# Kernel tuning notes

Hardware: AMD Instinct MI355X
Metric: run time of the kernel (lower is better)

Reference implementation:

```python
import jax, jax.numpy as jnp
import numpy as np

B, H, W, C = 1, 72, 72, 768
NH, HD = 12, 64
FF = 3072
EPS = 1e-6
THETA = 10000.0
S = H * W


def _rope_tables():
    freqs = 1.0 / THETA ** (np.arange(0, HD, 4, dtype=np.float32) / HD)  # [16]
    t = np.arange(H, dtype=np.float32)
    fx = np.outer(t, freqs)  # [72,16]
    fy = np.outer(t, freqs)
    fx = np.tile(fx[:, None, :], (1, W, 1))  # [72,72,16]
    fy = np.tile(fy[None, :, :], (H, 1, 1))
    fxy = np.concatenate([fx, fy], axis=-1).reshape(S, -1)  # [5184,32]
    fxy = np.repeat(fxy, 2, axis=-1)  # [5184,64]
    return jnp.asarray(np.cos(fxy)), jnp.asarray(np.sin(fxy))


def _rotate_pairwise(x):
    x1 = x[..., ::2]
    x2 = x[..., 1::2]
    return jnp.stack([-x2, x1], axis=-1).reshape(x.shape)


def _layernorm(x, g, b):
    m = jnp.mean(x, axis=-1, keepdims=True)
    v = jnp.mean(jnp.square(x - m), axis=-1, keepdims=True)
    return (x - m) * jax.lax.rsqrt(v + EPS) * g + b


def setup_inputs() -> dict:
    key = jax.random.key(0)
    ks = jax.random.split(key, 12)
    s_c = 1.0 / np.sqrt(C)
    s_ff = 1.0 / np.sqrt(FF)
    d = {
        "hidden_states": jax.random.normal(ks[0], (B, H, W, C), jnp.float32),
        "wq": jax.random.normal(ks[1], (C, C), jnp.float32) * s_c,
        "bq": jnp.zeros((C,), jnp.float32),
        "wk": jax.random.normal(ks[2], (C, C), jnp.float32) * s_c,
        "bk": jnp.zeros((C,), jnp.float32),
        "wv": jax.random.normal(ks[3], (C, C), jnp.float32) * s_c,
        "bv": jnp.zeros((C,), jnp.float32),
        "wo": jax.random.normal(ks[4], (C, C), jnp.float32) * s_c,
        "bo": jnp.zeros((C,), jnp.float32),
        "g1": jnp.ones((C,), jnp.float32),
        "b1": jnp.zeros((C,), jnp.float32),
        "g2": jnp.ones((C,), jnp.float32),
        "b2": jnp.zeros((C,), jnp.float32),
        "w_fc1": jax.random.normal(ks[5], (C, FF), jnp.float32) * s_c,
        "b_fc1": jnp.zeros((FF,), jnp.float32),
        "w_fc2": jax.random.normal(ks[6], (FF, C), jnp.float32) * s_ff,
        "b_fc2": jnp.zeros((C,), jnp.float32),
        "ls1": jnp.full((C,), 1e-5, jnp.float32),
        "ls2": jnp.full((C,), 1e-5, jnp.float32),
    }
    return d


def reference(hidden_states, wq, bq, wk, bk, wv, bv, wo, bo, g1, b1, g2, b2,
              w_fc1, b_fc1, w_fc2, b_fc2, ls1, ls2):
    cos, sin = _rope_tables()  # [S, HD]
    cos = cos[None, None]  # [1,1,S,HD]
    sin = sin[None, None]

    residual = hidden_states
    x = hidden_states.reshape(B, S, C)
    x = _layernorm(x, g1, b1)

    # attention
    q = (x @ wq + bq).reshape(B, S, NH, HD).transpose(0, 2, 1, 3)
    k = (x @ wk + bk).reshape(B, S, NH, HD).transpose(0, 2, 1, 3)
    v = (x @ wv + bv).reshape(B, S, NH, HD).transpose(0, 2, 1, 3)
    q = q * cos + _rotate_pairwise(q) * sin
    k = k * cos + _rotate_pairwise(k) * sin
    scale = HD ** -0.5
    attn = jax.nn.softmax(jnp.einsum('bhqd,bhkd->bhqk', q, k) * scale, axis=-1)
    o = jnp.einsum('bhqk,bhkd->bhqd', attn, v)
    o = o.transpose(0, 2, 1, 3).reshape(B, S, C)
    o = o @ wo + bo
    o = o * ls1

    hs = residual + o.reshape(B, H, W, C)
    residual = hs
    x = _layernorm(hs.reshape(B, S, C), g2, b2)
    x = jax.nn.gelu(x @ w_fc1 + b_fc1, approximate=False)
    x = x @ w_fc2 + b_fc2
    x = x * ls2
    return residual + x.reshape(B, H, W, C)
```

## Files before the change

### kernel.cpp

```cpp
#include <hip/hip_runtime.h>

#define S_  5184
#define C_  768
#define NH_ 12
#define HD_ 64
#define FF_ 3072
#define WW_ 72

typedef __attribute__((ext_vector_type(8))) short bf16x8;
typedef __attribute__((ext_vector_type(4))) float f32x4;

__device__ __forceinline__ float bf2f(unsigned short u){
    unsigned int i = ((unsigned int)u) << 16; float f; __builtin_memcpy(&f,&i,4); return f;
}
__device__ __forceinline__ unsigned short f2bf(float f){
    unsigned int i; __builtin_memcpy(&i,&f,4);
    unsigned int r = (i + 0x7fffu + ((i>>16)&1u)) >> 16;
    return (unsigned short)r;
}
__device__ __forceinline__ float ldf(float v){ return v; }
__device__ __forceinline__ float ldf(unsigned short v){ return bf2f(v); }

__device__ __forceinline__ void gload16(const void* g, const void* l) {
    __builtin_amdgcn_global_load_lds((const __attribute__((address_space(1))) void*)g,
                                     (__attribute__((address_space(3))) void*)l, 16, 0, 0);
}
__device__ __forceinline__ unsigned int cvtpk(float lo, float hi){
    unsigned int r;
    asm volatile("v_cvt_pk_bf16_f32 %0, %1, %2" : "=v"(r) : "v"(lo), "v"(hi));
    return r;
}

template<typename TIN>
__global__ __launch_bounds__(256) void ln_k(const TIN* __restrict__ x,
                                            const float* __restrict__ g,
                                            const float* __restrict__ b,
                                            unsigned short* __restrict__ out)
{
    int row = blockIdx.x, tid = threadIdx.x;
    const TIN* xr = x + (size_t)row * C_;
    float v0 = ldf(xr[tid]), v1 = ldf(xr[tid+256]), v2 = ldf(xr[tid+512]);
    float s = v0+v1+v2, q = v0*v0+v1*v1+v2*v2;
    #pragma unroll
    for (int off=32; off; off>>=1){ s += __shfl_xor(s,off); q += __shfl_xor(q,off); }
    __shared__ float ss[4], qq[4], mshare[2];
    int lane = tid & 63, wv = tid >> 6;
    if (!lane){ ss[wv] = s; qq[wv] = q; }
    __syncthreads();
    if (!tid){
        float S2 = ss[0]+ss[1]+ss[2]+ss[3];
        float Q2 = qq[0]+qq[1]+qq[2]+qq[3];
        float mean = S2 * (1.f/C_);
        float var  = Q2 * (1.f/C_) - mean*mean;
        mshare[0] = mean; mshare[1] = rsqrtf(var + 1e-6f);
    }
    __syncthreads();
    float mean = mshare[0], inv = mshare[1];
    unsigned short* orow = out + (size_t)row * C_;
    orow[tid]     = f2bf((v0-mean)*inv*g[tid]     + b[tid]);
    orow[tid+256] = f2bf((v1-mean)*inv*g[tid+256] + b[tid+256]);
    orow[tid+512] = f2bf((v2-mean)*inv*g[tid+512] + b[tid+512]);
}

__global__ __launch_bounds__(256) void rope_tables_k(float* __restrict__ cosT,
                                                     float* __restrict__ sinT)
{
    int idx = blockIdx.x * 256 + threadIdx.x;
    if (idx >= S_*32) return;
    int s = idx >> 5, i = idx & 31;
    int hh = s / WW_, ww = s % WW_;
    int m = i & 15;
    float coord = (i < 16) ? (float)hh : (float)ww;
    float freq = powf(10000.0f, -(float)m / 16.0f);
    float a = coord * freq;
    float c = cosf(a), sn = sinf(a);
    cosT[s*64 + 2*i]   = c;  cosT[s*64 + 2*i+1] = c;
    sinT[s*64 + 2*i]   = sn; sinT[s*64 + 2*i+1] = sn;
}

__global__ __launch_bounds__(256) void rope_apply_k(unsigned short* __restrict__ q,
                                                    unsigned short* __restrict__ k,
                                                    const float* __restrict__ cosT,
                                                    const float* __restrict__ sinT)
{
    int idx = blockIdx.x * 256 + threadIdx.x;
    if (idx >= S_*NH_*32) return;
    int s = idx / (NH_*32);
    int p = idx % (NH_*32);
    int h = p >> 5, i = p & 31;
    size_t base = (size_t)s*C_ + h*HD_ + 2*i;
    float c = cosT[s*64 + 2*i], sn = sinT[s*64 + 2*i];
    float x0 = bf2f(q[base]), x1 = bf2f(q[base+1]);
    q[base]   = f2bf((x0*c - x1*sn) * 0.125f);
    q[base+1] = f2bf((x1*c + x0*sn) * 0.125f);
    x0 = bf2f(k[base]); x1 = bf2f(k[base+1]);
    k[base]   = f2bf(x0*c - x1*sn);
    k[base+1] = f2bf(x1*c + x0*sn);
}

__global__ __launch_bounds__(256) void transpose_w(const float* __restrict__ W,
                                                   unsigned short* __restrict__ WT,
                                                   int K, int N)
{
    __shared__ float t[32][33];
    int tx = threadIdx.x, ty = threadIdx.y;
    int n0 = blockIdx.x * 32, k0 = blockIdx.y * 32;
    #pragma unroll
    for (int i = 0; i < 4; i++)
        t[ty + i*8][tx] = W[(size_t)(k0 + ty + i*8)*N + n0 + tx];
    __syncthreads();
    #pragma unroll
    for (int i = 0; i < 4; i++)
        WT[(size_t)(n0 + ty + i*8)*K + k0 + tx] = f2bf(t[tx][ty + i*8]);
}

template<int EPI, int NWC>
__global__ __launch_bounds__(256) void gemm_mfma(const unsigned short* __restrict__ A,
                                                 const unsigned short* __restrict__ BT,
                                                 const float* __restrict__ bias,
                                                 const float* __restrict__ biasB,
                                                 const float* __restrict__ biasC,
                                                 const float* __restrict__ scale,
                                                 const float* __restrict__ addend,
                                                 void* __restrict__ outp,
                                                 void* __restrict__ outp2,
                                                 int M, int N, int K)
{
    const int BN = 64*NWC;
    const int MI = (NWC == 2) ? 4 : 2;
    __shared__ __align__(16) unsigned short As[2][8192];
    __shared__ __align__(16) unsigned short Bs[2][4096*NWC];
    int tid = threadIdx.x;
    int w = tid >> 6, lane = tid & 63, lq = lane & 15, lk = lane >> 4;
    int wr = (NWC == 2) ? (w >> 1) : w;
    int wc = (NWC == 2) ? (w & 1) : 0;
    int bm = blockIdx.y * 128, bn = blockIdx.x * BN;

    f32x4 acc[MI][4];
    #pragma unroll
    for (int i = 0; i < MI; i++)
        #pragma unroll
        for (int j = 0; j < 4; j++) acc[i][j] = 0;

    auto STAGE = [&](int buf, int kt) {
        #pragma unroll
        for (int u = 0; u < 4; u++) {
            int t = w*4 + u;
            int c = t*64 + lane;
            int kg = c >> 7, row = c & 127;
            int ra = bm + row; if (ra >= M) ra = M - 1;
            gload16(A + (size_t)ra*K + kt*64 + kg*8, As[buf] + t*512);
        }
        #pragma unroll
        for (int u = 0; u < 2*NWC; u++) {
            int t = w*2*NWC + u;
            int c = t*64 + lane;
            int kg = (NWC == 2) ? (c >> 7) : (c >> 6);
            int row = (NWC == 2) ? (c & 127) : (c & 63);
            gload16(BT + (size_t)(bn + row)*K + kt*64 + kg*8, Bs[buf] + t*512);
        }
    };

    int nk = K / 64;
    STAGE(0, 0);
    int cur = 0;
    for (int kt = 0; kt < nk; kt++) {
        __syncthreads();
        if (kt + 1 < nk) STAGE(cur ^ 1, kt + 1);
        #pragma unroll
        for (int kk = 0; kk < 2; kk++) {
            bf16x8 af[MI], bfr[4];
            #pragma unroll
            for (int mi = 0; mi < MI; mi++)
                af[mi] = *(const bf16x8*)(As[cur] + (kk*4 + lk)*1024 + (wr*MI*16 + mi*16 + lq)*8);
            #pragma unroll
            for (int ni = 0; ni < 4; ni++)
                bfr[ni] = *(const bf16x8*)(Bs[cur] + (kk*4 + lk)*BN*8 + (wc*64 + ni*16 + lq)*8);
            #pragma unroll
            for (int mi = 0; mi < MI; mi++)
                #pragma unroll
                for (int ni = 0; ni < 4; ni++)
                    acc[mi][ni] = __builtin_amdgcn_mfma_f32_16x16x32_bf16(af[mi], bfr[ni], acc[mi][ni], 0, 0, 0);
        }
        cur ^= 1;
    }

    #pragma unroll
    for (int mi = 0; mi < MI; mi++) {
        #pragma unroll
        for (int ni = 0; ni < 4; ni++) {
            int n = bn + wc*64 + ni*16 + lq;
            int m0 = bm + wr*MI*16 + mi*16 + lk*4;
            if (EPI == 4) {
                if (n < 1536) {
                    const float* bb = (n < 768) ? bias : biasB;
                    int nn = (n < 768) ? n : (n - 768);
                    size_t base = (n < 768) ? 0 : ((size_t)S_ * 768);
                    #pragma unroll
                    for (int r = 0; r < 4; r++) {
                        int m = m0 + r;
                        if (m < M)
                            ((unsigned short*)outp)[base + (size_t)m*768 + nn] = f2bf(acc[mi][ni][r] + bb[nn]);
                    }
                } else {
                    if (m0 < M) {
                        float bv = biasC[n - 1536];
                        ushort4 pv;
                        pv.x = f2bf(acc[mi][ni][0] + bv);
                        pv.y = f2bf(acc[mi][ni][1] + bv);
                        pv.z = f2bf(acc[mi][ni][2] + bv);
                        pv.w = f2bf(acc[mi][ni][3] + bv);
                        *(ushort4*)((unsigned short*)outp2 + (size_t)(n - 1536)*S_ + m0) = pv;
                    }
                }
            } else {
                #pragma unroll
                for (int r = 0; r < 4; r++) {
                    int m = m0 + r;
                    if (m < M) {
                        float v = acc[mi][ni][r] + bias[n];
                        if (EPI == 1) {
                            v = 0.5f * v * (1.f + erff(v * 0.70710678f));
                            ((unsigned short*)outp)[(size_t)m*N + n] = f2bf(v);
                        } else {
                            size_t o = (size_t)m*N + n;
                            ((float*)outp)[o] = v*scale[n] + addend[o];
                        }
                    }
                }
            }
        }
    }
}

__global__ __launch_bounds__(256) void attn_mfma2(const unsigned short* __restrict__ Q,
                                                  const unsigned short* __restrict__ Kb,
                                                  const unsigned short* __restrict__ Vt,
                                                  unsigned short* __restrict__ O)
{
    __shared__ __align__(16) unsigned short Ks[2][4096];
    __shared__ __align__(16) unsigned short Vs[2][4096];
    int tid = threadIdx.x;
    int w = tid >> 6, lane = tid & 63, lq = lane & 15, lk = lane >> 4;
    int h = blockIdx.y;
    int q0 = blockIdx.x * 128 + w * 32;

    bf16x8 qf[2][2];
    #pragma unroll
    for (int qi = 0; qi < 2; qi++) {
        int qr = q0 + qi*16 + lq; if (qr >= S_) qr = S_ - 1;
        #pragma unroll
        for (int ks = 0; ks < 2; ks++)
            qf[qi][ks] = *(const bf16x8*)(Q + (size_t)qr*C_ + h*64 + ks*32 + lk*8);
    }

    f32x4 oacc[2][4];
    #pragma unroll
    for (int qi = 0; qi < 2; qi++)
        #pragma unroll
        for (int df = 0; df < 4; df++) oacc[qi][df] = 0;
    float m_[2] = {-INFINITY, -INFINITY};
    float l_[2] = {0.f, 0.f};

    auto STAGE = [&](int buf, int t) {
        int kv0 = t * 64;
        #pragma unroll
        for (int u = 0; u < 4; u++) {
            int tt = w*4 + u;
            if (tt < 8)
                gload16(Kb + (size_t)(kv0 + lane)*C_ + h*64 + tt*8, Ks[buf] + tt*512);
            else
                gload16(Vt + (size_t)(h*64 + lane)*S_ + kv0 + (tt-8)*8, Vs[buf] + (tt-8)*512);
        }
    };

    const int NT = S_/64;
    STAGE(0, 0);
    int cur = 0;
    for (int t = 0; t < NT; t++) {
        __syncthreads();
        if (t + 1 < NT) STAGE(cur ^ 1, t + 1);

        f32x4 s[2][4];
        #pragma unroll
        for (int qi = 0; qi < 2; qi++)
            #pragma unroll
            for (int nf = 0; nf < 4; nf++) s[qi][nf] = 0;
        #pragma unroll
        for (int ks = 0; ks < 2; ks++) {
            #pragma unroll
            for (int nf = 0; nf < 4; nf++) {
                bf16x8 kf = *(const bf16x8*)(Ks[cur] + (ks*4 + lk)*512 + (nf*16 + lq)*8);
                #pragma unroll
                for (int qi = 0; qi < 2; qi++)
                    s[qi][nf] = __builtin_amdgcn_mfma_f32_16x16x32_bf16(kf, qf[qi][ks], s[qi][nf], 0, 0, 0);
            }
        }

        unsigned int pk[2][8];
        #pragma unroll
        for (int qi = 0; qi < 2; qi++) {
            float tm = -INFINITY;
            #pragma unroll
            for (int nf = 0; nf < 4; nf++)
                #pragma unroll
                for (int r = 0; r < 4; r++) tm = fmaxf(tm, s[qi][nf][r]);
            tm = fmaxf(tm, __shfl_xor(tm, 16));
            tm = fmaxf(tm, __shfl_xor(tm, 32));
            float mn = fmaxf(m_[qi], tm);
            float corr = __expf(m_[qi] - mn);
            m_[qi] = mn;
            float ps = 0.f;
            #pragma unroll
            for (int nf = 0; nf < 4; nf++)
                #pragma unroll
                for (int r = 0; r < 4; r++) {
                    float p = __expf(s[qi][nf][r] - mn);
                    s[qi][nf][r] = p; ps += p;
                }
            ps += __shfl_xor(ps, 16);
            ps += __shfl_xor(ps, 32);
            l_[qi] = l_[qi]*corr + ps;
            #pragma unroll
            for (int df = 0; df < 4; df++)
                #pragma unroll
                for (int r = 0; r < 4; r++) oacc[qi][df][r] *= corr;
            #pragma unroll
            for (int nf = 0; nf < 4; nf++) {
                pk[qi][nf*2+0] = cvtpk(s[qi][nf][0], s[qi][nf][1]);
                pk[qi][nf*2+1] = cvtpk(s[qi][nf][2], s[qi][nf][3]);
            }
        }

        #pragma unroll
        for (int ks = 0; ks < 2; ks++) {
            #pragma unroll
            for (int df = 0; df < 4; df++) {
                int d = df*16 + lq;
                union { bf16x8 v; unsigned long long dd[2]; } va;
                va.dd[0] = *(const unsigned long long*)(Vs[cur] + (4*ks + (lk>>1))*512 + d*8 + (lk&1)*4);
                va.dd[1] = *(const unsigned long long*)(Vs[cur] + (4*ks + 2 + (lk>>1))*512 + d*8 + (lk&1)*4);
                #pragma unroll
                for (int qi = 0; qi < 2; qi++) {
                    union { bf16x8 v; unsigned int u[4]; } pb;
                    pb.u[0] = pk[qi][4*ks+0]; pb.u[1] = pk[qi][4*ks+1];
                    pb.u[2] = pk[qi][4*ks+2]; pb.u[3] = pk[qi][4*ks+3];
                    oacc[qi][df] = __builtin_amdgcn_mfma_f32_16x16x32_bf16(va.v, pb.v, oacc[qi][df], 0, 0, 0);
                }
            }
        }
        cur ^= 1;
    }

    #pragma unroll
    for (int qi = 0; qi < 2; qi++) {
        int q = q0 + qi*16 + lq;
        if (q < S_) {
            float rl = 1.f / l_[qi];
            #pragma unroll
            for (int df = 0; df < 4; df++) {
                ushort4 pv;
                pv.x = f2bf(oacc[qi][df][0] * rl);
                pv.y = f2bf(oacc[qi][df][1] * rl);
                pv.z = f2bf(oacc[qi][df][2] * rl);
                pv.w = f2bf(oacc[qi][df][3] * rl);
                *(ushort4*)(O + (size_t)q*C_ + h*64 + df*16 + lk*4) = pv;
            }
        }
    }
}

extern "C" void kernel_launch(void* const* d_in, const int* in_sizes, int n_in,
                              void* d_out, int out_size, void* d_ws, size_t ws_size,
                              hipStream_t stream)
{
    const float* hidden = (const float*)d_in[0];
    const float* wq  = (const float*)d_in[1];
    const float* bq  = (const float*)d_in[2];
    const float* wk  = (const float*)d_in[3];
    const float* bk  = (const float*)d_in[4];
    const float* wv  = (const float*)d_in[5];
    const float* bv  = (const float*)d_in[6];
    const float* wo  = (const float*)d_in[7];
    const float* bo  = (const float*)d_in[8];
    const float* g1  = (const float*)d_in[9];
    const float* b1  = (const float*)d_in[10];
    const float* g2  = (const float*)d_in[11];
    const float* b2  = (const float*)d_in[12];
    const float* wf1 = (const float*)d_in[13];
    const float* bf1 = (const float*)d_in[14];
    const float* wf2 = (const float*)d_in[15];
    const float* bf2_ = (const float*)d_in[16];
    const float* ls1 = (const float*)d_in[17];
    const float* ls2 = (const float*)d_in[18];

    char* ws = (char*)d_ws;
    size_t off = 0;
    auto alloc = [&](size_t bytes) { char* p = ws + off; off += (bytes + 255) & ~(size_t)255; return p; };

    float* res1          = (float*)alloc((size_t)S_*C_*4);
    float* cosT          = (float*)alloc((size_t)S_*64*4);
    float* sinT          = (float*)alloc((size_t)S_*64*4);
    unsigned short* lnb  = (unsigned short*)alloc((size_t)S_*C_*2);
    unsigned short* qb   = (unsigned short*)alloc((size_t)S_*C_*2);
    unsigned short* kb   = (unsigned short*)alloc((size_t)S_*C_*2);
    unsigned short* vtb  = (unsigned short*)alloc((size_t)S_*C_*2);
    unsigned short* ob   = (unsigned short*)alloc((size_t)S_*C_*2);
    unsigned short* fc1b = qb;
    unsigned short* wqT  = (unsigned short*)alloc((size_t)C_*C_*2);
    unsigned short* wkT  = (unsigned short*)alloc((size_t)C_*C_*2);
    unsigned short* wvT  = (unsigned short*)alloc((size_t)C_*C_*2);
    unsigned short* woT  = (unsigned short*)alloc((size_t)C_*C_*2);
    unsigned short* wf1T = (unsigned short*)alloc((size_t)C_*FF_*2);
    unsigned short* wf2T = (unsigned short*)alloc((size_t)C_*FF_*2);
    float* outb = (float*)d_out;

    hipLaunchKernelGGL(transpose_w, dim3(C_/32, C_/32), dim3(32,8), 0, stream, wq,  wqT,  C_, C_);
    hipLaunchKernelGGL(transpose_w, dim3(C_/32, C_/32), dim3(32,8), 0, stream, wk,  wkT,  C_, C_);
    hipLaunchKernelGGL(transpose_w, dim3(C_/32, C_/32), dim3(32,8), 0, stream, wv,  wvT,  C_, C_);
    hipLaunchKernelGGL(transpose_w, dim3(C_/32, C_/32), dim3(32,8), 0, stream, wo,  woT,  C_, C_);
    hipLaunchKernelGGL(transpose_w, dim3(FF_/32, C_/32), dim3(32,8), 0, stream, wf1, wf1T, C_, FF_);
    hipLaunchKernelGGL(transpose_w, dim3(C_/32, FF_/32), dim3(32,8), 0, stream, wf2, wf2T, FF_, C_);
    hipLaunchKernelGGL(ln_k<float>, dim3(S_), dim3(256), 0, stream, hidden, g1, b1, lnb);
    hipLaunchKernelGGL(rope_tables_k, dim3((S_*32 + 255)/256), dim3(256), 0, stream, cosT, sinT);
    hipLaunchKernelGGL((gemm_mfma<4,2>), dim3(2304/128, 41), dim3(256), 0, stream,
                       lnb, wqT, bq, bk, bv, (const float*)nullptr, (const float*)nullptr,
                       (void*)qb, (void*)vtb, S_, 2304, C_);
    hipLaunchKernelGGL(rope_apply_k, dim3((S_*NH_*32 + 255)/256), dim3(256), 0, stream,
                       qb, kb, cosT, sinT);
    hipLaunchKernelGGL(attn_mfma2, dim3((S_ + 127)/128, NH_), dim3(256), 0, stream, qb, kb, vtb, ob);
    hipLaunchKernelGGL((gemm_mfma<2,1>), dim3(C_/64, 41), dim3(256), 0, stream,
                       ob, woT, bo, (const float*)nullptr, (const float*)nullptr, ls1, hidden,
                       (void*)res1, (void*)nullptr, S_, C_, C_);
    hipLaunchKernelGGL(ln_k<float>, dim3(S_), dim3(256), 0, stream, res1, g2, b2, lnb);
    hipLaunchKernelGGL((gemm_mfma<1,2>), dim3(FF_/128, 41), dim3(256), 0, stream,
                       lnb, wf1T, bf1, (const float*)nullptr, (const float*)nullptr,
                       (const float*)nullptr, (const float*)nullptr,
                       (void*)fc1b, (void*)nullptr, S_, FF_, C_);
    hipLaunchKernelGGL((gemm_mfma<2,1>), dim3(C_/64, 41), dim3(256), 0, stream,
                       fc1b, wf2T, bf2_, (const float*)nullptr, (const float*)nullptr, ls2, res1,
                       (void*)outb, (void*)nullptr, S_, C_, FF_);
    (void)in_sizes; (void)n_in; (void)out_size; (void)ws_size;
}
```

Baseline: 477.8 us.

## Split attention over KV halves, fuse rope and transposes, remap GEMM blocks by XCD

Attention now splits the key range into two halves across a third grid dimension, writing partial outputs plus max and sum values that a new combine kernel merges. This gives more workgroups to fill the GPU, in exchange for extra memory traffic and one more launch. The change also computes RoPE angles inline and drops the cos/sin tables. It merges the six weight transposes into one launch and remaps GEMM block IDs so neighbouring tiles share an XCD. The softmax moves to exp2 with the log2e factor folded into the Q scale, skips the rescale when the running max does not change, and raises wave priority around the MFMA sections.

Result: slower. 499.1 us (+4.4%).

```diff
diff --git a/kernel.cpp b/kernel.cpp
--- a/kernel.cpp
+++ b/kernel.cpp
@@ -62,8 +62,8 @@
     orow[tid+512] = f2bf((v2-mean)*inv*g[tid+512] + b[tid+512]);
 }
 
-__global__ __launch_bounds__(256) void rope_tables_k(float* __restrict__ cosT,
-                                                     float* __restrict__ sinT)
+__global__ __launch_bounds__(256) void rope_k(unsigned short* __restrict__ q,
+                                              unsigned short* __restrict__ k)
 {
     int idx = blockIdx.x * 256 + threadIdx.x;
     if (idx >= S_*32) return;
@@ -74,37 +74,38 @@
     float freq = powf(10000.0f, -(float)m / 16.0f);
     float a = coord * freq;
     float c = cosf(a), sn = sinf(a);
-    cosT[s*64 + 2*i]   = c;  cosT[s*64 + 2*i+1] = c;
-    sinT[s*64 + 2*i]   = sn; sinT[s*64 + 2*i+1] = sn;
-}
-
-__global__ __launch_bounds__(256) void rope_apply_k(unsigned short* __restrict__ q,
-                                                    unsigned short* __restrict__ k,
-                                                    const float* __restrict__ cosT,
-                                                    const float* __restrict__ sinT)
-{
-    int idx = blockIdx.x * 256 + threadIdx.x;
-    if (idx >= S_*NH_*32) return;
-    int s = idx / (NH_*32);
-    int p = idx % (NH_*32);
-    int h = p >> 5, i = p & 31;
-    size_t base = (size_t)s*C_ + h*HD_ + 2*i;
-    float c = cosT[s*64 + 2*i], sn = sinT[s*64 + 2*i];
-    float x0 = bf2f(q[base]), x1 = bf2f(q[base+1]);
-    q[base]   = f2bf((x0*c - x1*sn) * 0.125f);
-    q[base+1] = f2bf((x1*c + x0*sn) * 0.125f);
-    x0 = bf2f(k[base]); x1 = bf2f(k[base+1]);
-    k[base]   = f2bf(x0*c - x1*sn);
-    k[base+1] = f2bf(x1*c + x0*sn);
-}
-
-__global__ __launch_bounds__(256) void transpose_w(const float* __restrict__ W,
-                                                   unsigned short* __restrict__ WT,
-                                                   int K, int N)
+    const float QS = 0.18033688011112042f;
+    #pragma unroll
+    for (int h = 0; h < NH_; h++) {
+        size_t base = (size_t)s*C_ + h*HD_ + 2*i;
+        float x0 = bf2f(q[base]), x1 = bf2f(q[base+1]);
+        q[base]   = f2bf((x0*c - x1*sn) * QS);
+        q[base+1] = f2bf((x1*c + x0*sn) * QS);
+        x0 = bf2f(k[base]); x1 = bf2f(k[base+1]);
+        k[base]   = f2bf(x0*c - x1*sn);
+        k[base+1] = f2bf(x1*c + x0*sn);
+    }
+}
+
+__global__ __launch_bounds__(256) void transpose_all(const float* __restrict__ wq, unsigned short* __restrict__ wqT,
+                                                     const float* __restrict__ wk, unsigned short* __restrict__ wkT,
+                                                     const float* __restrict__ wv, unsigned short* __restrict__ wvT,
+                                                     const float* __restrict__ wo, unsigned short* __restrict__ woT,
+                                                     const float* __restrict__ wf1, unsigned short* __restrict__ wf1T,
+                                                     const float* __restrict__ wf2, unsigned short* __restrict__ wf2T)
 {
     __shared__ float t[32][33];
-    int tx = threadIdx.x, ty = threadIdx.y;
-    int n0 = blockIdx.x * 32, k0 = blockIdx.y * 32;
+    int b = blockIdx.x;
+    const float* W; unsigned short* WT; int K, N, tb;
+    if      (b < 576)  { W = wq;  WT = wqT;  K = 768;  N = 768;  tb = b; }
+    else if (b < 1152) { W = wk;  WT = wkT;  K = 768;  N = 768;  tb = b - 576; }
+    else if (b < 1728) { W = wv;  WT = wvT;  K = 768;  N = 768;  tb = b - 1152; }
+    else if (b < 2304) { W = wo;  WT = woT;  K = 768;  N = 768;  tb = b - 1728; }
+    else if (b < 4608) { W = wf1; WT = wf1T; K = 768;  N = 3072; tb = b - 2304; }
+    else               { W = wf2; WT = wf2T; K = 3072; N = 768;  tb = b - 4608; }
+    int ntx = N / 32;
+    int n0 = (tb % ntx) * 32, k0 = (tb / ntx) * 32;
+    int tx = threadIdx.x & 31, ty = threadIdx.x >> 5;
     #pragma unroll
     for (int i = 0; i < 4; i++)
         t[ty + i*8][tx] = W[(size_t)(k0 + ty + i*8)*N + n0 + tx];
@@ -134,7 +135,14 @@
     int w = tid >> 6, lane = tid & 63, lq = lane & 15, lk = lane >> 4;
     int wr = (NWC == 2) ? (w >> 1) : w;
     int wc = (NWC == 2) ? (w & 1) : 0;
-    int bm = blockIdx.y * 128, bn = blockIdx.x * BN;
+
+    int gx = gridDim.x;
+    int nwg = gx * gridDim.y;
+    int bid = blockIdx.y * gx + blockIdx.x;
+    int xcd = bid & 7, idx = bid >> 3;
+    int qq = nwg >> 3, rr = nwg & 7;
+    int wg = (xcd < rr) ? (xcd*(qq+1) + idx) : (rr*(qq+1) + (xcd-rr)*qq + idx);
+    int bm = (wg / gx) * 128, bn = (wg % gx) * BN;
 
     f32x4 acc[MI][4];
     #pragma unroll
@@ -233,16 +241,18 @@
     }
 }
 
-__global__ __launch_bounds__(256) void attn_mfma2(const unsigned short* __restrict__ Q,
+__global__ __launch_bounds__(256) void attn_split(const unsigned short* __restrict__ Q,
                                                   const unsigned short* __restrict__ Kb,
                                                   const unsigned short* __restrict__ Vt,
-                                                  unsigned short* __restrict__ O)
+                                                  unsigned short* __restrict__ po,
+                                                  float* __restrict__ pm,
+                                                  float* __restrict__ pl)
 {
     __shared__ __align__(16) unsigned short Ks[2][4096];
     __shared__ __align__(16) unsigned short Vs[2][4096];
     int tid = threadIdx.x;
     int w = tid >> 6, lane = tid & 63, lq = lane & 15, lk = lane >> 4;
-    int h = blockIdx.y;
+    int h = blockIdx.y, half = blockIdx.z;
     int q0 = blockIdx.x * 128 + w * 32;
 
     bf16x8 qf[2][2];
@@ -275,17 +285,20 @@
     };
 
     const int NT = S_/64;
-    STAGE(0, 0);
+    int t0 = half * ((NT + 1) / 2);
+    int t1 = (half == 0) ? ((NT + 1) / 2) : NT;
+    STAGE(0, t0);
     int cur = 0;
-    for (int t = 0; t < NT; t++) {
+    for (int t = t0; t < t1; t++) {
         __syncthreads();
-        if (t + 1 < NT) STAGE(cur ^ 1, t + 1);
+        if (t + 1 < t1) STAGE(cur ^ 1, t + 1);
 
         f32x4 s[2][4];
         #pragma unroll
         for (int qi = 0; qi < 2; qi++)
             #pragma unroll
             for (int nf = 0; nf < 4; nf++) s[qi][nf] = 0;
+        __builtin_amdgcn_s_setprio(1);
         #pragma unroll
         for (int ks = 0; ks < 2; ks++) {
             #pragma unroll
@@ -296,6 +309,7 @@
                     s[qi][nf] = __builtin_amdgcn_mfma_f32_16x16x32_bf16(kf, qf[qi][ks], s[qi][nf], 0, 0, 0);
             }
         }
+        __builtin_amdgcn_s_setprio(0);
 
         unsigned int pk[2][8];
         #pragma unroll
@@ -307,24 +321,27 @@
                 for (int r = 0; r < 4; r++) tm = fmaxf(tm, s[qi][nf][r]);
             tm = fmaxf(tm, __shfl_xor(tm, 16));
             tm = fmaxf(tm, __shfl_xor(tm, 32));
-            float mn = fmaxf(m_[qi], tm);
-            float corr = __expf(m_[qi] - mn);
-            m_[qi] = mn;
+            if (__any(tm > m_[qi])) {
+                float mn = fmaxf(m_[qi], tm);
+                float corr = exp2f(m_[qi] - mn);
+                m_[qi] = mn;
+                l_[qi] *= corr;
+                #pragma unroll
+                for (int df = 0; df < 4; df++)
+                    #pragma unroll
+                    for (int r = 0; r < 4; r++) oacc[qi][df][r] *= corr;
+            }
             float ps = 0.f;
             #pragma unroll
             for (int nf = 0; nf < 4; nf++)
                 #pragma unroll
                 for (int r = 0; r < 4; r++) {
-                    float p = __expf(s[qi][nf][r] - mn);
+                    float p = exp2f(s[qi][nf][r] - m_[qi]);
                     s[qi][nf][r] = p; ps += p;
                 }
             ps += __shfl_xor(ps, 16);
             ps += __shfl_xor(ps, 32);
-            l_[qi] = l_[qi]*corr + ps;
-            #pragma unroll
-            for (int df = 0; df < 4; df++)
-                #pragma unroll
-                for (int r = 0; r < 4; r++) oacc[qi][df][r] *= corr;
+            l_[qi] += ps;
             #pragma unroll
             for (int nf = 0; nf < 4; nf++) {
                 pk[qi][nf*2+0] = cvtpk(s[qi][nf][0], s[qi][nf][1]);
@@ -332,6 +349,7 @@
             }
         }
 
+        __builtin_amdgcn_s_setprio(1);
         #pragma unroll
         for (int ks = 0; ks < 2; ks++) {
             #pragma unroll
@@ -349,9 +367,11 @@
                 }
             }
         }
+        __builtin_amdgcn_s_setprio(0);
         cur ^= 1;
     }
 
+    size_t hb = (size_t)half * S_;
     #pragma unroll
     for (int qi = 0; qi < 2; qi++) {
         int q = q0 + qi*16 + lq;
@@ -364,10 +384,42 @@
                 pv.y = f2bf(oacc[qi][df][1] * rl);
                 pv.z = f2bf(oacc[qi][df][2] * rl);
                 pv.w = f2bf(oacc[qi][df][3] * rl);
-                *(ushort4*)(O + (size_t)q*C_ + h*64 + df*16 + lk*4) = pv;
-            }
-        }
-    }
+                *(ushort4*)(po + (hb + q)*C_ + h*64 + df*16 + lk*4) = pv;
+            }
+            if (lk == 0) {
+                pm[(hb + q)*NH_ + h] = m_[qi];
+                pl[(hb + q)*NH_ + h] = l_[qi];
+            }
+        }
+    }
+}
+
+__global__ __launch_bounds__(256) void attn_combine(const unsigned short* __restrict__ po,
+                                                    const float* __restrict__ pm,
+                                                    const float* __restrict__ pl,
+                                                    unsigned short* __restrict__ O)
+{
+    int gid = blockIdx.x * 256 + threadIdx.x;
+    if (gid >= S_*NH_*16) return;
+    int chunk = gid & 15;
+    int pair = gid >> 4;
+    int h = pair % NH_, q = pair / NH_;
+    float m1 = pm[(size_t)q*NH_ + h],        l1 = pl[(size_t)q*NH_ + h];
+    float m2 = pm[((size_t)S_ + q)*NH_ + h], l2 = pl[((size_t)S_ + q)*NH_ + h];
+    float M = fmaxf(m1, m2);
+    float w1 = l1 * exp2f(m1 - M), w2 = l2 * exp2f(m2 - M);
+    float rd = 1.f / (w1 + w2);
+    w1 *= rd; w2 *= rd;
+    size_t o1 = (size_t)q*C_ + h*64 + chunk*4;
+    size_t o2 = ((size_t)S_ + q)*C_ + h*64 + chunk*4;
+    ushort4 a = *(const ushort4*)(po + o1);
+    ushort4 b = *(const ushort4*)(po + o2);
+    ushort4 out;
+    out.x = f2bf(w1*bf2f(a.x) + w2*bf2f(b.x));
+    out.y = f2bf(w1*bf2f(a.y) + w2*bf2f(b.y));
+    out.z = f2bf(w1*bf2f(a.z) + w2*bf2f(b.z));
+    out.w = f2bf(w1*bf2f(a.w) + w2*bf2f(b.w));
+    *(ushort4*)(O + o1) = out;
 }
 
 extern "C" void kernel_launch(void* const* d_in, const int* in_sizes, int n_in,
@@ -399,8 +451,6 @@
     auto alloc = [&](size_t bytes) { char* p = ws + off; off += (bytes + 255) & ~(size_t)255; return p; };
 
     float* res1          = (float*)alloc((size_t)S_*C_*4);
-    float* cosT          = (float*)alloc((size_t)S_*64*4);
-    float* sinT          = (float*)alloc((size_t)S_*64*4);
     unsigned short* lnb  = (unsigned short*)alloc((size_t)S_*C_*2);
     unsigned short* qb   = (unsigned short*)alloc((size_t)S_*C_*2);
     unsigned short* kb   = (unsigned short*)alloc((size_t)S_*C_*2);
@@ -415,20 +465,21 @@
     unsigned short* wf2T = (unsigned short*)alloc((size_t)C_*FF_*2);
     float* outb = (float*)d_out;
 
-    hipLaunchKernelGGL(transpose_w, dim3(C_/32, C_/32), dim3(32,8), 0, stream, wq,  wqT,  C_, C_);
-    hipLaunchKernelGGL(transpose_w, dim3(C_/32, C_/32), dim3(32,8), 0, stream, wk,  wkT,  C_, C_);
-    hipLaunchKernelGGL(transpose_w, dim3(C_/32, C_/32), dim3(32,8), 0, stream, wv,  wvT,  C_, C_);
-    hipLaunchKernelGGL(transpose_w, dim3(C_/32, C_/32), dim3(32,8), 0, stream, wo,  woT,  C_, C_);
-    hipLaunchKernelGGL(transpose_w, dim3(FF_/32, C_/32), dim3(32,8), 0, stream, wf1, wf1T, C_, FF_);
-    hipLaunchKernelGGL(transpose_w, dim3(C_/32, FF_/32), dim3(32,8), 0, stream, wf2, wf2T, FF_, C_);
-    hipLaunchKernelGGL(ln_k<float>, dim3(S_), dim3(256), 0, stream, hidden, g1, b1, lnb);
-    hipLaunchKernelGGL(rope_tables_k, dim3((S_*32 + 255)/256), dim3(256), 0, stream, cosT, sinT);
+    unsigned short* po = (unsigned short*)res1;
+    float* pm = (float*)lnb;
+    float* pl = pm + (size_t)2*S_*NH_;
+
+    hipLaunchKernelGGL(transpose_all, dim3(6912), dim3(256), 0, stream,
+                       wq, wqT, wk, wkT, wv, wvT, wo, woT, wf1, wf1T, wf2, wf2T);
+    hipLaunchKernelGGL(ln_k<float>, dim3(S_), dim3(256), 0, stream, hidden, g1, b1, lnb + (size_t)0);
     hipLaunchKernelGGL((gemm_mfma<4,2>), dim3(2304/128, 41), dim3(256), 0, stream,
                        lnb, wqT, bq, bk, bv, (const float*)nullptr, (const float*)nullptr,
                        (void*)qb, (void*)vtb, S_, 2304, C_);
-    hipLaunchKernelGGL(rope_apply_k, dim3((S_*NH_*32 + 255)/256), dim3(256), 0, stream,
-                       qb, kb, cosT, sinT);
-    hipLaunchKernelGGL(attn_mfma2, dim3((S_ + 127)/128, NH_), dim3(256), 0, stream, qb, kb, vtb, ob);
+    hipLaunchKernelGGL(rope_k, dim3((S_*32 + 255)/256), dim3(256), 0, stream, qb, kb);
+    hipLaunchKernelGGL(attn_split, dim3((S_ + 127)/128, NH_, 2), dim3(256), 0, stream,
+                       qb, kb, vtb, po, pm, pl);
+    hipLaunchKernelGGL(attn_combine, dim3((S_*NH_*16 + 255)/256), dim3(256), 0, stream,
+                       po, pm, pl, ob);
     hipLaunchKernelGGL((gemm_mfma<2,1>), dim3(C_/64, 41), dim3(256), 0, stream,
                        ob, woT, bo, (const float*)nullptr, (const float*)nullptr, ls1, hidden,
                        (void*)res1, (void*)nullptr, S_, C_, C_);
```
